# Optimization experiments

Hardware: AMD Instinct MI355X
Metric: run time of the kernel (lower is better)

## Reference

```python
import jax, jax.numpy as jnp
import numpy as np

B, IN, H, OUT = 8192, 2048, 2048, 512
DEG = 4            # polynomial_degree -> DEG+1 basis functions
BN_EPS = 1e-5


def setup_inputs() -> dict:
    key = jax.random.key(0)
    ks = jax.random.split(key, 8)
    inv_in = 1.0 / np.sqrt(IN)
    inv_h = 1.0 / np.sqrt(H)
    inv_deg = 1.0 / (IN * (DEG + 1))
    return {
        "x": jax.random.normal(ks[0], (B, IN), jnp.float32),
        "w1_base": jax.random.normal(ks[1], (H, IN), jnp.float32) * inv_in,
        "b1_base": jnp.zeros((H,), jnp.float32),
        "c1": jax.random.normal(ks[2], (IN, H, DEG + 1), jnp.float32) * inv_deg,
        "s1": jnp.ones((H,), jnp.float32),
        "bn_gamma": jnp.ones((H,), jnp.float32),
        "bn_beta": jnp.zeros((H,), jnp.float32),
        "w2_base": jax.random.normal(ks[3], (OUT, H), jnp.float32) * inv_h,
        "b2_base": jnp.zeros((OUT,), jnp.float32),
        "c2": jax.random.normal(ks[4], (H, OUT, DEG + 1), jnp.float32) * (1.0 / (H * (DEG + 1))),
        "s2": jnp.ones((OUT,), jnp.float32),
    }


def _cheby_kan_linear(x, w_base, b_base, coeffs, scaler):
    # Base linear path (skip_activation=True -> no SiLU on x).
    base = x @ w_base.T + b_base                      # [B, out]
    # tanh normalization into [-1, 1] for Chebyshev domain.
    xn = jnp.tanh(x)                                  # [B, in]
    Ts = [jnp.ones_like(xn), xn]
    for _ in range(DEG - 1):
        Ts.append(2.0 * xn * Ts[-1] - Ts[-2])
    T = jnp.stack(Ts, axis=-1)                        # [B, in, DEG+1]
    poly = jnp.einsum('bid,iod->bo', T, coeffs)       # [B, out]
    return base + poly * scaler


def _batchnorm1d(x, gamma, beta):
    # Training-mode BatchNorm1d: biased batch statistics over the batch axis.
    mu = jnp.mean(x, axis=0)
    var = jnp.var(x, axis=0)
    return gamma * (x - mu) * jax.lax.rsqrt(var + BN_EPS) + beta


def reference(x, w1_base, b1_base, c1, s1, bn_gamma, bn_beta,
              w2_base, b2_base, c2, s2):
    h = _cheby_kan_linear(x, w1_base, b1_base, c1, s1)
    h = _batchnorm1d(h, bn_gamma, bn_beta)
    return _cheby_kan_linear(h, w2_base, b2_base, c2, s2)
```

## Files before the change

### kernel.cpp

```cpp
#include <hip/hip_runtime.h>
#include <hip/hip_bf16.h>

#define NB   8192
#define NI   2048
#define NH   2048
#define NO   512
#define KP   10240
#define CHNK 4096
#define BNEPS 1e-5f

typedef short bf16x8 __attribute__((ext_vector_type(8)));
typedef float f32x4 __attribute__((ext_vector_type(4)));
typedef unsigned int u32_g __attribute__((address_space(1)));
typedef unsigned int u32_l __attribute__((address_space(3)));

__device__ __forceinline__ void load_lds16(const void* g, void* l) {
  __builtin_amdgcn_global_load_lds((const u32_g*)g, (u32_l*)l, 16, 0, 0);
}

__device__ __forceinline__ unsigned short f2bf(float f) {
  __hip_bfloat16 h = __float2bfloat16(f);
  unsigned short u;
  __builtin_memcpy(&u, &h, 2);
  return u;
}

__global__ __launch_bounds__(256) void build_w_kernel(
    const float* __restrict__ wbase, const float* __restrict__ coef,
    const float* __restrict__ scaler, __hip_bfloat16* __restrict__ Wp,
    float* __restrict__ acc, int Nout, int Kin)
{
  __shared__ float lds0[64][65];
  __shared__ __hip_bfloat16 ldsT[64][4][68];
  const int t = threadIdx.x;
  const int o0 = blockIdx.x * 64;
  const int i0 = blockIdx.y * 64;

  for (int r = t; r < 64 * 64 * 5; r += 256) {
    int li = r / 320;
    int rem = r - li * 320;
    int lo = rem / 5;
    int d = rem - lo * 5;
    float v = coef[((size_t)(i0 + li) * Nout + (o0 + lo)) * 5 + d];
    if (d == 0) lds0[lo][li] = v;
    else        ldsT[lo][d - 1][li] = __float2bfloat16(v);
  }
  __syncthreads();

  const size_t Kw = (size_t)5 * Kin;
  for (int r = t; r < 64 * 4 * 64; r += 256) {
    int li = r & 63;
    int d  = (r >> 6) & 3;
    int lo = r >> 8;
    float v = __bfloat162float(ldsT[lo][d][li]) * scaler[o0 + lo];
    Wp[(size_t)(o0 + lo) * Kw + (size_t)(d + 1) * Kin + i0 + li] = __float2bfloat16(v);
  }
  for (int r = t; r < 64 * 64; r += 256) {
    int li = r & 63;
    int lo = r >> 6;
    Wp[(size_t)(o0 + lo) * Kw + i0 + li] =
        __float2bfloat16(wbase[(size_t)(o0 + lo) * Kin + i0 + li]);
  }
  {
    int lo = t >> 2, q = t & 3;
    float s = 0.f;
    #pragma unroll
    for (int j = 0; j < 16; ++j) s += lds0[lo][q * 16 + j];
    s += __shfl_xor(s, 1);
    s += __shfl_xor(s, 2);
    if (q == 0) atomicAdd(&acc[o0 + lo], s);
  }
}

__global__ __launch_bounds__(256) void build_a1_kernel(
    const float* __restrict__ x, __hip_bfloat16* __restrict__ Ap, int b0)
{
  const size_t idx = ((size_t)blockIdx.x * 256 + threadIdx.x) * 4;
  const size_t row = idx >> 11;
  const int i = (int)(idx & 2047);
  const float4 xv = *(const float4*)(x + (size_t)b0 * NI + idx);
  const float xa[4] = {xv.x, xv.y, xv.z, xv.w};
  unsigned short u0[4], u1[4], u2[4], u3[4], u4[4];
  #pragma unroll
  for (int j = 0; j < 4; ++j) {
    float v  = xa[j];
    float tn = tanhf(v);
    float t2 = fmaf(2.f * tn, tn, -1.f);
    float t3 = fmaf(2.f * tn, t2, -tn);
    float t4 = fmaf(2.f * tn, t3, -t2);
    u0[j] = f2bf(v);  u1[j] = f2bf(tn); u2[j] = f2bf(t2);
    u3[j] = f2bf(t3); u4[j] = f2bf(t4);
  }
  __hip_bfloat16* bp = Ap + row * KP + i;
  *(ushort4*)(bp)          = make_ushort4(u0[0], u0[1], u0[2], u0[3]);
  *(ushort4*)(bp + NI)     = make_ushort4(u1[0], u1[1], u1[2], u1[3]);
  *(ushort4*)(bp + 2 * NI) = make_ushort4(u2[0], u2[1], u2[2], u2[3]);
  *(ushort4*)(bp + 3 * NI) = make_ushort4(u3[0], u3[1], u3[2], u3[3]);
  *(ushort4*)(bp + 4 * NI) = make_ushort4(u4[0], u4[1], u4[2], u4[3]);
}

__global__ __launch_bounds__(256) void build_a2_kernel(
    const __hip_bfloat16* __restrict__ h, const float* __restrict__ mu,
    const float* __restrict__ rsig, const float* __restrict__ gam,
    const float* __restrict__ bet, __hip_bfloat16* __restrict__ Ap, int b0)
{
  const size_t idx = ((size_t)blockIdx.x * 256 + threadIdx.x) * 4;
  const size_t row = idx >> 11;
  const int j0 = (int)(idx & 2047);
  const ushort4 hv = *(const ushort4*)(h + (size_t)b0 * NH + idx);
  const float4 muv = *(const float4*)(mu + j0);
  const float4 rsv = *(const float4*)(rsig + j0);
  const float4 gv  = *(const float4*)(gam + j0);
  const float4 bv  = *(const float4*)(bet + j0);
  unsigned short hu[4] = {hv.x, hv.y, hv.z, hv.w};
  const float ma[4] = {muv.x, muv.y, muv.z, muv.w};
  const float ra[4] = {rsv.x, rsv.y, rsv.z, rsv.w};
  const float ga[4] = {gv.x, gv.y, gv.z, gv.w};
  const float ba[4] = {bv.x, bv.y, bv.z, bv.w};
  unsigned short u0[4], u1[4], u2[4], u3[4], u4[4];
  #pragma unroll
  for (int j = 0; j < 4; ++j) {
    __hip_bfloat16 hb;
    __builtin_memcpy(&hb, &hu[j], 2);
    float hv_f = __bfloat162float(hb);
    float hn = fmaf(ga[j] * (hv_f - ma[j]), ra[j], ba[j]);
    float tn = tanhf(hn);
    float t2 = fmaf(2.f * tn, tn, -1.f);
    float t3 = fmaf(2.f * tn, t2, -tn);
    float t4 = fmaf(2.f * tn, t3, -t2);
    u0[j] = f2bf(hn); u1[j] = f2bf(tn); u2[j] = f2bf(t2);
    u3[j] = f2bf(t3); u4[j] = f2bf(t4);
  }
  __hip_bfloat16* bp = Ap + row * KP + j0;
  *(ushort4*)(bp)          = make_ushort4(u0[0], u0[1], u0[2], u0[3]);
  *(ushort4*)(bp + NH)     = make_ushort4(u1[0], u1[1], u1[2], u1[3]);
  *(ushort4*)(bp + 2 * NH) = make_ushort4(u2[0], u2[1], u2[2], u2[3]);
  *(ushort4*)(bp + 3 * NH) = make_ushort4(u3[0], u3[1], u3[2], u3[3]);
  *(ushort4*)(bp + 4 * NH) = make_ushort4(u4[0], u4[1], u4[2], u4[3]);
}

__global__ __launch_bounds__(256) void bn_stats_kernel(
    const __hip_bfloat16* __restrict__ h, float* __restrict__ psum,
    float* __restrict__ psq)
{
  const int col = blockIdx.x * 256 + threadIdx.x;
  const int r0 = blockIdx.y * 256;
  float s = 0.f, q = 0.f;
  for (int r = 0; r < 256; ++r) {
    float v = __bfloat162float(h[(size_t)(r0 + r) * NH + col]);
    s += v;
    q = fmaf(v, v, q);
  }
  psum[(size_t)blockIdx.y * NH + col] = s;
  psq [(size_t)blockIdx.y * NH + col] = q;
}

__global__ __launch_bounds__(256) void bn_finalize_kernel(
    const float* __restrict__ psum, const float* __restrict__ psq,
    float* __restrict__ mu, float* __restrict__ rsig)
{
  const int j = blockIdx.x * 256 + threadIdx.x;
  float s = 0.f, q = 0.f;
  for (int c = 0; c < 32; ++c) {
    s += psum[(size_t)c * NH + j];
    q += psq [(size_t)c * NH + j];
  }
  const float invB = 1.f / (float)NB;
  float m = s * invB;
  float var = fmaf(q, invB, -m * m);
  mu[j] = m;
  rsig[j] = rsqrtf(var + BNEPS);
}

__global__ __launch_bounds__(256) void bias_init_kernel(
    float* __restrict__ out, const float* __restrict__ bb,
    const float* __restrict__ bs, const float* __restrict__ bacc)
{
  const size_t idx = ((size_t)blockIdx.x * 256 + threadIdx.x) * 4;
  const int col = (int)(idx & (NO - 1));
  const float4 b = *(const float4*)(bb + col);
  const float4 s = *(const float4*)(bs + col);
  const float4 a = *(const float4*)(bacc + col);
  float4 o;
  o.x = b.x + s.x * a.x; o.y = b.y + s.y * a.y;
  o.z = b.z + s.z * a.z; o.w = b.w + s.w * a.w;
  *(float4*)(out + idx) = o;
}

template<bool ATOMIC>
__global__ __launch_bounds__(256, 2) void gemm_db(
    const __hip_bfloat16* __restrict__ A, const __hip_bfloat16* __restrict__ Bm,
    void* __restrict__ Cv, const float* __restrict__ bb,
    const float* __restrict__ bs, const float* __restrict__ bacc,
    int N, int K, int nt, int lg2bps)
{
  __shared__ __attribute__((aligned(16))) __hip_bfloat16 As[2][128][64];
  __shared__ __attribute__((aligned(16))) __hip_bfloat16 Bs[2][128][64];
  const int tid  = threadIdx.x;
  const int lane = tid & 63;
  const int w    = tid >> 6;
  int swz = ((int)blockIdx.x & 7) * ((int)gridDim.x >> 3) + ((int)blockIdx.x >> 3);
  int k0 = 0;
  if constexpr (ATOMIC) {
    const int split = swz >> lg2bps;
    swz &= (1 << lg2bps) - 1;
    k0 = split * (nt * 64);
  }
  const int nTN = N >> 7;
  const int m0 = (swz / nTN) * 128;
  const int n0 = (swz % nTN) * 128;
  const int wr = (w >> 1) * 64;
  const int wc = (w & 1) * 64;

  const int srow = lane >> 3;
  const int scol = (((lane & 7) ^ srow) * 8);
  const __hip_bfloat16* Ag = A  + (size_t)(m0 + w * 32 + srow) * K + k0 + scol;
  const __hip_bfloat16* Bg = Bm + (size_t)(n0 + w * 32 + srow) * K + k0 + scol;

  f32x4 acc[4][4];
  #pragma unroll
  for (int m = 0; m < 4; ++m)
    #pragma unroll
    for (int n = 0; n < 4; ++n) {
      f32x4 z = {0.f, 0.f, 0.f, 0.f};
      acc[m][n] = z;
    }

  const int fr = lane & 15;
  const int kg = (lane >> 4) * 8;
  const int swz_r = (fr & 7) * 8;

  #define STAGE(buf, kt)                                                     \
    do {                                                                     \
      _Pragma("unroll")                                                      \
      for (int c = 0; c < 4; ++c)                                            \
        load_lds16(Ag + (size_t)c * 8 * K + (kt), &As[buf][w * 32 + c * 8][0]); \
      _Pragma("unroll")                                                      \
      for (int c = 0; c < 4; ++c)                                            \
        load_lds16(Bg + (size_t)c * 8 * K + (kt), &Bs[buf][w * 32 + c * 8][0]); \
    } while (0)

  STAGE(0, 0);
  STAGE(1, 64);
  asm volatile("s_waitcnt vmcnt(8)" ::: "memory");
  __builtin_amdgcn_s_barrier();

  for (int it = 0; it < nt; ++it) {
    const int cur = it & 1;
    bf16x8 af[4][2], bfr[4][2];
    #pragma unroll
    for (int m = 0; m < 4; ++m)
      #pragma unroll
      for (int kk = 0; kk < 2; ++kk)
        af[m][kk] = *(const bf16x8*)&As[cur][wr + m * 16 + fr][(kk * 32 + kg) ^ swz_r];
    #pragma unroll
    for (int n = 0; n < 4; ++n)
      #pragma unroll
      for (int kk = 0; kk < 2; ++kk)
        bfr[n][kk] = *(const bf16x8*)&Bs[cur][wc + n * 16 + fr][(kk * 32 + kg) ^ swz_r];
    asm volatile("s_waitcnt lgkmcnt(0)" ::: "memory");
    __builtin_amdgcn_s_barrier();
    const bool pre = (it + 2 < nt);
    if (pre) STAGE(cur, (it + 2) * 64);
    __builtin_amdgcn_s_setprio(1);
    #pragma unroll
    for (int m = 0; m < 4; ++m)
      #pragma unroll
      for (int n = 0; n < 4; ++n)
        #pragma unroll
        for (int kk = 0; kk < 2; ++kk)
          acc[m][n] = __builtin_amdgcn_mfma_f32_16x16x32_bf16(
              af[m][kk], bfr[n][kk], acc[m][n], 0, 0, 0);
    __builtin_amdgcn_s_setprio(0);
    if (pre) asm volatile("s_waitcnt vmcnt(8)" ::: "memory");
    else     asm volatile("s_waitcnt vmcnt(0)" ::: "memory");
    __builtin_amdgcn_s_barrier();
  }
  #undef STAGE

  const int cr = (lane >> 4) * 4;
  const int cc = lane & 15;
  if constexpr (ATOMIC) {
    float* C = (float*)Cv;
    #pragma unroll
    for (int n = 0; n < 4; ++n) {
      const int col = n0 + wc + n * 16 + cc;
      #pragma unroll
      for (int m = 0; m < 4; ++m) {
        float* Cp = C + (size_t)(m0 + wr + m * 16 + cr) * N + col;
        #pragma unroll
        for (int r = 0; r < 4; ++r)
          atomicAdd(&Cp[(size_t)r * N], acc[m][n][r]);
      }
    }
  } else {
    __hip_bfloat16* C = (__hip_bfloat16*)Cv;
    #pragma unroll
    for (int n = 0; n < 4; ++n) {
      const int col = n0 + wc + n * 16 + cc;
      const float bias = bb[col] + bs[col] * bacc[col];
      #pragma unroll
      for (int m = 0; m < 4; ++m) {
        __hip_bfloat16* Cp = C + (size_t)(m0 + wr + m * 16 + cr) * N + col;
        #pragma unroll
        for (int r = 0; r < 4; ++r)
          Cp[(size_t)r * N] = __float2bfloat16(acc[m][n][r] + bias);
      }
    }
  }
}

extern "C" void kernel_launch(void* const* d_in, const int* in_sizes, int n_in,
                              void* d_out, int out_size, void* d_ws, size_t ws_size,
                              hipStream_t stream) {
  (void)in_sizes; (void)n_in; (void)out_size;
  const float* x   = (const float*)d_in[0];
  const float* w1  = (const float*)d_in[1];
  const float* b1  = (const float*)d_in[2];
  const float* c1  = (const float*)d_in[3];
  const float* s1  = (const float*)d_in[4];
  const float* gam = (const float*)d_in[5];
  const float* bet = (const float*)d_in[6];
  const float* w2  = (const float*)d_in[7];
  const float* b2  = (const float*)d_in[8];
  const float* c2  = (const float*)d_in[9];
  const float* s2  = (const float*)d_in[10];
  float* out = (float*)d_out;

  const bool full = ws_size >= 243820544ULL;
  const size_t apBytes = full ? 167772160ULL : 83886080ULL;
  char* ws = (char*)d_ws;
  __hip_bfloat16* Ap = (__hip_bfloat16*)ws;
  __hip_bfloat16* Wp = (__hip_bfloat16*)(ws + apBytes);
  __hip_bfloat16* hb = (__hip_bfloat16*)(ws + apBytes + 41943040ULL);
  char* tail = ws + apBytes + 41943040ULL + 33554432ULL;
  float* acc1 = (float*)(tail);
  float* acc2 = (float*)(tail + 8192);
  float* psum = (float*)(tail + 10240);
  float* psq  = (float*)(tail + 272384);
  float* mu   = (float*)(tail + 534528);
  float* rsig = (float*)(tail + 542720);

  dim3 blk(256);
  hipMemsetAsync(acc1, 0, 8192 + 2048, stream);

  build_w_kernel<<<dim3(NH / 64, NI / 64), blk, 0, stream>>>(w1, c1, s1, Wp, acc1, NH, NI);

  if (full) {
    build_a1_kernel<<<(NB * NI / 4) / 256, blk, 0, stream>>>(x, Ap, 0);
    gemm_db<false><<<(NB / 128) * (NH / 128), blk, 0, stream>>>(
        Ap, Wp, hb, b1, s1, acc1, NH, KP, KP / 64, 0);
  } else {
    for (int ch = 0; ch < 2; ++ch) {
      int b0 = ch * CHNK;
      build_a1_kernel<<<(CHNK * NI / 4) / 256, blk, 0, stream>>>(x, Ap, b0);
      gemm_db<false><<<(CHNK / 128) * (NH / 128), blk, 0, stream>>>(
          Ap, Wp, hb + (size_t)b0 * NH, b1, s1, acc1, NH, KP, KP / 64, 0);
    }
  }

  bn_stats_kernel<<<dim3(NH / 256, 32), blk, 0, stream>>>(hb, psum, psq);
  bn_finalize_kernel<<<NH / 256, blk, 0, stream>>>(psum, psq, mu, rsig);

  build_w_kernel<<<dim3(NO / 64, NH / 64), blk, 0, stream>>>(w2, c2, s2, Wp, acc2, NO, NH);

  bias_init_kernel<<<(NB * NO / 4) / 256, blk, 0, stream>>>(out, b2, s2, acc2);

  if (full) {
    build_a2_kernel<<<(NB * NH / 4) / 256, blk, 0, stream>>>(hb, mu, rsig, gam, bet, Ap, 0);
    gemm_db<true><<<4 * (NB / 128) * (NO / 128), blk, 0, stream>>>(
        Ap, Wp, out, nullptr, nullptr, nullptr, NO, KP, (KP / 4) / 64, 8);
  } else {
    for (int ch = 0; ch < 2; ++ch) {
      int b0 = ch * CHNK;
      build_a2_kernel<<<(CHNK * NH / 4) / 256, blk, 0, stream>>>(hb, mu, rsig, gam, bet, Ap, b0);
      gemm_db<true><<<4 * (CHNK / 128) * (NO / 128), blk, 0, stream>>>(
          Ap, Wp, out + (size_t)b0 * NO, nullptr, nullptr, nullptr, NO, KP, (KP / 4) / 64, 7);
    }
  }
}
```

Measured before the change: 907.0 us.

## Use 256x256 eight-wave GEMM tile and replace atomic split-K with two-way partial reduce

The first GEMM moves from a 128x128 tile with 4 waves to a 256x256 tile with 8 waves (512 threads, one block per CU), so each wave computes an 8x4 grid of MFMA fragments and more data is reused per LDS load. The second GEMM goes from 4-way split-K with fp32 atomicAdd into the output to 2-way split-K. Each split writes a plain partial buffer, and a separate reduce kernel sums the two partials and adds the bias. The changes are meant to cut global/LDS traffic per FLOP and to remove atomic contention. In exchange, occupancy drops, register pressure rises, and the partial buffers add an extra write and read pass.

```diff
diff --git a/kernel.cpp b/kernel.cpp
--- a/kernel.cpp
+++ b/kernel.cpp
@@ -172,27 +172,135 @@
   rsig[j] = rsqrtf(var + BNEPS);
 }
 
-__global__ __launch_bounds__(256) void bias_init_kernel(
-    float* __restrict__ out, const float* __restrict__ bb,
-    const float* __restrict__ bs, const float* __restrict__ bacc)
+__global__ __launch_bounds__(256) void reduce2_kernel(
+    const float* __restrict__ p, float* __restrict__ out,
+    const float* __restrict__ bb, const float* __restrict__ bs,
+    const float* __restrict__ bacc, int rows)
 {
   const size_t idx = ((size_t)blockIdx.x * 256 + threadIdx.x) * 4;
   const int col = (int)(idx & (NO - 1));
-  const float4 b = *(const float4*)(bb + col);
-  const float4 s = *(const float4*)(bs + col);
-  const float4 a = *(const float4*)(bacc + col);
+  const float4 a = *(const float4*)(p + idx);
+  const float4 b = *(const float4*)(p + (size_t)rows * NO + idx);
+  const float4 bbv = *(const float4*)(bb + col);
+  const float4 bsv = *(const float4*)(bs + col);
+  const float4 bav = *(const float4*)(bacc + col);
   float4 o;
-  o.x = b.x + s.x * a.x; o.y = b.y + s.y * a.y;
-  o.z = b.z + s.z * a.z; o.w = b.w + s.w * a.w;
+  o.x = a.x + b.x + bbv.x + bsv.x * bav.x;
+  o.y = a.y + b.y + bbv.y + bsv.y * bav.y;
+  o.z = a.z + b.z + bbv.z + bsv.z * bav.z;
+  o.w = a.w + b.w + bbv.w + bsv.w * bav.w;
   *(float4*)(out + idx) = o;
 }
 
-template<bool ATOMIC>
-__global__ __launch_bounds__(256, 2) void gemm_db(
+__global__ __launch_bounds__(512, 1) void gemm_8w(
     const __hip_bfloat16* __restrict__ A, const __hip_bfloat16* __restrict__ Bm,
-    void* __restrict__ Cv, const float* __restrict__ bb,
+    __hip_bfloat16* __restrict__ C, const float* __restrict__ bb,
     const float* __restrict__ bs, const float* __restrict__ bacc,
-    int N, int K, int nt, int lg2bps)
+    int N, int K, int nit)
+{
+  __shared__ __attribute__((aligned(16))) __hip_bfloat16 As[2][256][64];
+  __shared__ __attribute__((aligned(16))) __hip_bfloat16 Bs[2][256][64];
+  const int tid  = threadIdx.x;
+  const int lane = tid & 63;
+  const int w    = tid >> 6;
+  const int swz = ((int)blockIdx.x & 7) * ((int)gridDim.x >> 3) + ((int)blockIdx.x >> 3);
+  const int nTN = N >> 8;
+  const int m0 = (swz / nTN) * 256;
+  const int n0 = (swz % nTN) * 256;
+  const int wrow = (w >> 2) * 128;
+  const int wcol = (w & 3) * 64;
+
+  const int srow = lane >> 3;
+  const int scol = ((lane & 7) ^ srow) * 8;
+  const __hip_bfloat16* Ag = A  + (size_t)(m0 + w * 8 + srow) * K + scol;
+  const __hip_bfloat16* Bg = Bm + (size_t)(n0 + w * 8 + srow) * K + scol;
+
+  f32x4 acc[8][4];
+  #pragma unroll
+  for (int m = 0; m < 8; ++m)
+    #pragma unroll
+    for (int n = 0; n < 4; ++n) {
+      f32x4 z = {0.f, 0.f, 0.f, 0.f};
+      acc[m][n] = z;
+    }
+
+  const int fr = lane & 15;
+  const int kg = (lane >> 4) * 8;
+  const int swz_r = (fr & 7) * 8;
+
+  #define STAGE8(buf, kt)                                                      \
+    do {                                                                       \
+      _Pragma("unroll")                                                        \
+      for (int c = 0; c < 4; ++c)                                              \
+        load_lds16(Ag + (size_t)(c * 64) * K + (kt), &As[buf][w * 8 + c * 64][0]); \
+      _Pragma("unroll")                                                        \
+      for (int c = 0; c < 4; ++c)                                              \
+        load_lds16(Bg + (size_t)(c * 64) * K + (kt), &Bs[buf][w * 8 + c * 64][0]); \
+    } while (0)
+
+  #define KTILE(BUF, DOSTAGE, KTS)                                             \
+    do {                                                                       \
+      _Pragma("unroll")                                                        \
+      for (int kk = 0; kk < 2; ++kk) {                                         \
+        bf16x8 bfr[4], af[8];                                                  \
+        _Pragma("unroll")                                                      \
+        for (int n = 0; n < 4; ++n)                                            \
+          bfr[n] = *(const bf16x8*)&Bs[BUF][wcol + n * 16 + fr][(kk * 32 + kg) ^ swz_r]; \
+        _Pragma("unroll")                                                      \
+        for (int m = 0; m < 8; ++m)                                            \
+          af[m] = *(const bf16x8*)&As[BUF][wrow + m * 16 + fr][(kk * 32 + kg) ^ swz_r]; \
+        if (kk == 1) {                                                         \
+          asm volatile("s_waitcnt lgkmcnt(0)" ::: "memory");                   \
+          __builtin_amdgcn_s_barrier();                                        \
+          if (DOSTAGE) STAGE8(BUF, KTS);                                       \
+        }                                                                      \
+        __builtin_amdgcn_s_setprio(1);                                         \
+        _Pragma("unroll")                                                      \
+        for (int m = 0; m < 8; ++m)                                            \
+          _Pragma("unroll")                                                    \
+          for (int n = 0; n < 4; ++n)                                          \
+            acc[m][n] = __builtin_amdgcn_mfma_f32_16x16x32_bf16(               \
+                af[m], bfr[n], acc[m][n], 0, 0, 0);                            \
+        __builtin_amdgcn_s_setprio(0);                                         \
+      }                                                                        \
+      if (DOSTAGE) asm volatile("s_waitcnt vmcnt(8)" ::: "memory");            \
+      else         asm volatile("s_waitcnt vmcnt(0)" ::: "memory");            \
+      __builtin_amdgcn_s_barrier();                                            \
+    } while (0)
+
+  STAGE8(0, 0);
+  STAGE8(1, 64);
+  asm volatile("s_waitcnt vmcnt(8)" ::: "memory");
+  __builtin_amdgcn_s_barrier();
+
+  for (int i = 0; i < nit; ++i) {
+    const int kts = (2 * i + 2) * 64;
+    const bool ds = (i + 1 < nit);
+    KTILE(0, ds, kts);
+    KTILE(1, ds, kts + 64);
+  }
+  #undef KTILE
+  #undef STAGE8
+
+  const int cr = (lane >> 4) * 4;
+  const int cc = lane & 15;
+  #pragma unroll
+  for (int n = 0; n < 4; ++n) {
+    const int col = n0 + wcol + n * 16 + cc;
+    const float bias = bb[col] + bs[col] * bacc[col];
+    #pragma unroll
+    for (int m = 0; m < 8; ++m) {
+      __hip_bfloat16* Cp = C + (size_t)(m0 + wrow + m * 16 + cr) * N + col;
+      #pragma unroll
+      for (int r = 0; r < 4; ++r)
+        Cp[(size_t)r * N] = __float2bfloat16(acc[m][n][r] + bias);
+    }
+  }
+}
+
+__global__ __launch_bounds__(256, 2) void gemm_sp(
+    const __hip_bfloat16* __restrict__ A, const __hip_bfloat16* __restrict__ Bm,
+    float* __restrict__ P, int M, int N, int K, int nt, int lg2bps)
 {
   __shared__ __attribute__((aligned(16))) __hip_bfloat16 As[2][128][64];
   __shared__ __attribute__((aligned(16))) __hip_bfloat16 Bs[2][128][64];
@@ -200,12 +308,9 @@
   const int lane = tid & 63;
   const int w    = tid >> 6;
   int swz = ((int)blockIdx.x & 7) * ((int)gridDim.x >> 3) + ((int)blockIdx.x >> 3);
-  int k0 = 0;
-  if constexpr (ATOMIC) {
-    const int split = swz >> lg2bps;
-    swz &= (1 << lg2bps) - 1;
-    k0 = split * (nt * 64);
-  }
+  const int split = swz >> lg2bps;
+  swz &= (1 << lg2bps) - 1;
+  const int k0 = split * (nt * 64);
   const int nTN = N >> 7;
   const int m0 = (swz / nTN) * 128;
   const int n0 = (swz % nTN) * 128;
@@ -280,32 +385,16 @@
 
   const int cr = (lane >> 4) * 4;
   const int cc = lane & 15;
-  if constexpr (ATOMIC) {
-    float* C = (float*)Cv;
-    #pragma unroll
-    for (int n = 0; n < 4; ++n) {
-      const int col = n0 + wc + n * 16 + cc;
+  float* Pb = P + (size_t)split * M * N;
+  #pragma unroll
+  for (int n = 0; n < 4; ++n) {
+    const int col = n0 + wc + n * 16 + cc;
+    #pragma unroll
+    for (int m = 0; m < 4; ++m) {
+      float* Pp = Pb + (size_t)(m0 + wr + m * 16 + cr) * N + col;
       #pragma unroll
-      for (int m = 0; m < 4; ++m) {
-        float* Cp = C + (size_t)(m0 + wr + m * 16 + cr) * N + col;
-        #pragma unroll
-        for (int r = 0; r < 4; ++r)
-          atomicAdd(&Cp[(size_t)r * N], acc[m][n][r]);
-      }
-    }
-  } else {
-    __hip_bfloat16* C = (__hip_bfloat16*)Cv;
-    #pragma unroll
-    for (int n = 0; n < 4; ++n) {
-      const int col = n0 + wc + n * 16 + cc;
-      const float bias = bb[col] + bs[col] * bacc[col];
-      #pragma unroll
-      for (int m = 0; m < 4; ++m) {
-        __hip_bfloat16* Cp = C + (size_t)(m0 + wr + m * 16 + cr) * N + col;
-        #pragma unroll
-        for (int r = 0; r < 4; ++r)
-          Cp[(size_t)r * N] = __float2bfloat16(acc[m][n][r] + bias);
-      }
+      for (int r = 0; r < 4; ++r)
+        Pp[(size_t)r * N] = acc[m][n][r];
     }
   }
 }
@@ -333,6 +422,7 @@
   __hip_bfloat16* Ap = (__hip_bfloat16*)ws;
   __hip_bfloat16* Wp = (__hip_bfloat16*)(ws + apBytes);
   __hip_bfloat16* hb = (__hip_bfloat16*)(ws + apBytes + 41943040ULL);
+  float* pbuf = (float*)hb;
   char* tail = ws + apBytes + 41943040ULL + 33554432ULL;
   float* acc1 = (float*)(tail);
   float* acc2 = (float*)(tail + 8192);
@@ -342,20 +432,21 @@
   float* rsig = (float*)(tail + 542720);
 
   dim3 blk(256);
+  dim3 blk512(512);
   hipMemsetAsync(acc1, 0, 8192 + 2048, stream);
 
   build_w_kernel<<<dim3(NH / 64, NI / 64), blk, 0, stream>>>(w1, c1, s1, Wp, acc1, NH, NI);
 
   if (full) {
     build_a1_kernel<<<(NB * NI / 4) / 256, blk, 0, stream>>>(x, Ap, 0);
-    gemm_db<false><<<(NB / 128) * (NH / 128), blk, 0, stream>>>(
-        Ap, Wp, hb, b1, s1, acc1, NH, KP, KP / 64, 0);
+    gemm_8w<<<(NB / 256) * (NH / 256), blk512, 0, stream>>>(
+        Ap, Wp, hb, b1, s1, acc1, NH, KP, KP / 128);
   } else {
     for (int ch = 0; ch < 2; ++ch) {
       int b0 = ch * CHNK;
       build_a1_kernel<<<(CHNK * NI / 4) / 256, blk, 0, stream>>>(x, Ap, b0);
-      gemm_db<false><<<(CHNK / 128) * (NH / 128), blk, 0, stream>>>(
-          Ap, Wp, hb + (size_t)b0 * NH, b1, s1, acc1, NH, KP, KP / 64, 0);
+      gemm_8w<<<(CHNK / 256) * (NH / 256), blk512, 0, stream>>>(
+          Ap, Wp, hb + (size_t)b0 * NH, b1, s1, acc1, NH, KP, KP / 128);
     }
   }
 
@@ -364,18 +455,20 @@
 
   build_w_kernel<<<dim3(NO / 64, NH / 64), blk, 0, stream>>>(w2, c2, s2, Wp, acc2, NO, NH);
 
-  bias_init_kernel<<<(NB * NO / 4) / 256, blk, 0, stream>>>(out, b2, s2, acc2);
-
   if (full) {
     build_a2_kernel<<<(NB * NH / 4) / 256, blk, 0, stream>>>(hb, mu, rsig, gam, bet, Ap, 0);
-    gemm_db<true><<<4 * (NB / 128) * (NO / 128), blk, 0, stream>>>(
-        Ap, Wp, out, nullptr, nullptr, nullptr, NO, KP, (KP / 4) / 64, 8);
+    gemm_sp<<<2 * (NB / 128) * (NO / 128), blk, 0, stream>>>(
+        Ap, Wp, pbuf, NB, NO, KP, (KP / 2) / 64, 8);
+    reduce2_kernel<<<(NB * NO / 4) / 256, blk, 0, stream>>>(
+        pbuf, out, b2, s2, acc2, NB);
   } else {
     for (int ch = 0; ch < 2; ++ch) {
       int b0 = ch * CHNK;
       build_a2_kernel<<<(CHNK * NH / 4) / 256, blk, 0, stream>>>(hb, mu, rsig, gam, bet, Ap, b0);
-      gemm_db<true><<<4 * (CHNK / 128) * (NO / 128), blk, 0, stream>>>(
-          Ap, Wp, out + (size_t)b0 * NO, nullptr, nullptr, nullptr, NO, KP, (KP / 4) / 64, 7);
-    }
-  }
-}
+      gemm_sp<<<2 * (CHNK / 128) * (NO / 128), blk, 0, stream>>>(
+          Ap, Wp, pbuf, CHNK, NO, KP, (KP / 2) / 64, 7);
+      reduce2_kernel<<<(CHNK * NO / 4) / 256, blk, 0, stream>>>(
+          pbuf, out + (size_t)b0 * NO, b2, s2, acc2, CHNK);
+    }
+  }
+}
```

Measured after the change: 1.010 ms. +11.4%, slower.
